# Kernel optimization log

Hardware: AMD Instinct MI355X
Metric: run time of the kernel (lower is better)

Reference implementation:

```python
import jax, jax.numpy as jnp
import numpy as np

NBINS = 128
LOGSCALE = False


def setup_inputs() -> dict:
    key = jax.random.key(0)
    X = jax.random.normal(key, (2048, 32768), dtype=jnp.float32)
    return {"X": X}


def reference(X) -> jnp.ndarray:
    # Flatten all non-leading dims (mirrors X.view(len(X), -1))
    X = X.reshape(X.shape[0], -1)
    ns = X.shape[1]
    nfreqs = 2 * (NBINS - 1) + 1          # window length (255)
    hop = nfreqs // 2
    starts = jnp.arange(0, ns - nfreqs + 1, hop)          # [nwin]
    idx = starts[:, None] + jnp.arange(nfreqs)[None, :]    # [nwin, nfreqs]
    W = X[:, idx]                          # [ntrials, nwin, nfreqs] gathered windows
    # One batched rfft + fused |.|^2 and mean over windows (Welch average)
    S = jnp.mean(jnp.abs(jnp.fft.rfft(W, axis=-1)) ** 2, axis=1)  # [ntrials, NBINS]
    if LOGSCALE:
        S = jnp.log10(S)
    return S
```

## Files before the change

kernel.cpp:

```cpp
#include <hip/hip_runtime.h>
#include <hip/hip_bf16.h>

#define NS     32768
#define NROWS  2048
#define HOP    127
#define NW     257
#define NB     128
#define WTILE  16
#define NT     17
#define TWOPI_255 0.02463994236f

typedef _Float16 f16;
typedef __attribute__((ext_vector_type(8))) _Float16 f16x8;
typedef __attribute__((ext_vector_type(4))) float f32x4;

__device__ inline f32x4 load4u(const float* p) {
    f32x4 v;
    __builtin_memcpy(&v, p, 16);
    return v;
}

__global__ __launch_bounds__(256, 4)
void psd_kernel(const float* __restrict__ X, float* __restrict__ out) {
    const int row  = blockIdx.x;
    const int tid  = threadIdx.x;
    const int lane = tid & 63;
    const int cq   = tid >> 6;
    const int r16  = lane & 15;
    const int kg   = lane >> 4;
    const int is_sin = cq >> 1;

    __shared__ alignas(16) f16 atile[2][WTILE * 256];
    __shared__ float scol[256];

    const float* __restrict__ xrow = X + (size_t)row * NS;

    const int sw  = tid >> 4;
    const int sk0 = (tid & 15) * 8;

    f32x4 fva, fvb, rva, rvb;
    {
        const int b = sw * HOP;
        fva = load4u(xrow + b + sk0);
        fvb = load4u(xrow + b + sk0 + 4);
        rva = load4u(xrow + b + 248 - sk0);
        rvb = load4u(xrow + b + 252 - sk0);
    }

    f16x8 bfrag[4][4];
    #pragma unroll
    for (int nt = 0; nt < 4; ++nt) {
        const int comp = cq * 64 + nt * 16 + r16;
        const int f    = comp & 127;
        #pragma unroll
        for (int kk = 0; kk < 4; ++kk) {
            int m = (f * (kk * 32 + kg * 8)) % 255;
            f16x8 v;
            #pragma unroll
            for (int j = 0; j < 8; ++j) {
                const float ang = (float)m * TWOPI_255;
                const float s   = is_sin ? __sinf(ang) : __cosf(ang);
                v[j] = (f16)s;
                m += f; if (m >= 255) m -= 255;
            }
            bfrag[nt][kk] = v;
        }
    }

    const f16x8 z8 = {(f16)0,(f16)0,(f16)0,(f16)0,(f16)0,(f16)0,(f16)0,(f16)0};
    auto fold_write = [&](int buf, bool valid) {
        float yp[8], ym[8];
        #pragma unroll
        for (int j = 0; j < 8; ++j) {
            const float fj = (j < 4) ? fva[j] : fvb[j - 4];
            const int   pi = 7 - j;
            const float rj = (pi < 4) ? rva[pi] : rvb[pi - 4];
            yp[j] = fj + rj;
            ym[j] = fj - rj;
        }
        if (sk0 == 0) { yp[0] = fva[0]; ym[0] = 0.0f; }
        f16x8 h0, h1;
        #pragma unroll
        for (int j = 0; j < 8; ++j) { h0[j] = (f16)yp[j]; h1[j] = (f16)ym[j]; }
        if (!valid) { h0 = z8; h1 = z8; }
        char* wp = (char*)&atile[buf][0];
        const uint sb  = (uint)(sw * 512 + sk0 * 2);
        const uint swz = (uint)((sw & 7) << 4);
        *(f16x8*)(wp + (sb ^ swz))         = h0;
        *(f16x8*)(wp + ((sb + 256) ^ swz)) = h1;
    };

    fold_write(0, true);
    {
        const int b = (WTILE + sw) * HOP;
        fva = load4u(xrow + b + sk0);
        fvb = load4u(xrow + b + sk0 + 4);
        rva = load4u(xrow + b + 248 - sk0);
        rvb = load4u(xrow + b + 252 - sk0);
    }
    __syncthreads();

    float ssum[4] = {0.f, 0.f, 0.f, 0.f};
    const uint rswz  = (uint)((r16 & 7) << 4);
    const uint rbase = (uint)(r16 * 512 + is_sin * 256 + kg * 16);

    for (int mt = 0; mt < NT; ++mt) {
        const int cur = mt & 1;

        const char* ap = (const char*)&atile[cur][0];
        f32x4 acc0 = {0,0,0,0}, acc1 = {0,0,0,0}, acc2 = {0,0,0,0}, acc3 = {0,0,0,0};
        __builtin_amdgcn_s_setprio(1);
        #pragma unroll
        for (int kk = 0; kk < 4; ++kk) {
            const f16x8 af = *(const f16x8*)(ap + ((rbase + (uint)(kk * 64)) ^ rswz));
            acc0 = __builtin_amdgcn_mfma_f32_16x16x32_f16(af, bfrag[0][kk], acc0, 0, 0, 0);
            acc1 = __builtin_amdgcn_mfma_f32_16x16x32_f16(af, bfrag[1][kk], acc1, 0, 0, 0);
            acc2 = __builtin_amdgcn_mfma_f32_16x16x32_f16(af, bfrag[2][kk], acc2, 0, 0, 0);
            acc3 = __builtin_amdgcn_mfma_f32_16x16x32_f16(af, bfrag[3][kk], acc3, 0, 0, 0);
        }
        __builtin_amdgcn_s_setprio(0);
        #pragma unroll
        for (int r = 0; r < 4; ++r) {
            ssum[0] += acc0[r] * acc0[r];
            ssum[1] += acc1[r] * acc1[r];
            ssum[2] += acc2[r] * acc2[r];
            ssum[3] += acc3[r] * acc3[r];
        }

        if (mt < NT - 1) {
            const bool valid = ((mt + 1) * WTILE + sw) < NW;
            fold_write(cur ^ 1, valid);
        }
        if (mt < NT - 2) {
            const int w = (mt + 2) * WTILE + sw;
            int b = w * HOP; if (b > NS - 256) b = NS - 256;
            fva = load4u(xrow + b + sk0);
            fvb = load4u(xrow + b + sk0 + 4);
            rva = load4u(xrow + b + 248 - sk0);
            rvb = load4u(xrow + b + 252 - sk0);
        }
        __syncthreads();
    }

    #pragma unroll
    for (int nt = 0; nt < 4; ++nt) {
        float v = ssum[nt];
        v += __shfl_xor(v, 16, 64);
        v += __shfl_xor(v, 32, 64);
        if (kg == 0) scol[cq * 64 + nt * 16 + r16] = v;
    }
    __syncthreads();
    if (tid < NB) {
        out[(size_t)row * NB + tid] = (scol[tid] + scol[tid + NB]) * (1.0f / 257.0f);
    }
}

extern "C" void kernel_launch(void* const* d_in, const int* in_sizes, int n_in,
                              void* d_out, int out_size, void* d_ws, size_t ws_size,
                              hipStream_t stream) {
    const float* X = (const float*)d_in[0];
    float* out = (float*)d_out;
    (void)in_sizes; (void)n_in; (void)d_ws; (void)ws_size; (void)out_size;
    psd_kernel<<<dim3(NROWS), dim3(256), 0, stream>>>(X, out);
}
```

Baseline: 65.09 us.

## Prefetch next A fragments into registers and overlap fold with MFMA

Restructures the main loop so the next tile's fold and LDS write, the global prefetch and the barrier all happen before the current tile's MFMAs. The A fragments for the next tile are read into registers ahead of time, so the MFMAs run from registers while LDS traffic and global loads are in flight. The fold now converts to packed fp16 first and does the add and subtract in packed half precision, which slightly changes rounding. The full __syncthreads is replaced by an LDS-only waitcnt plus barrier, and the occupancy hint drops from 4 to 3 blocks to leave room for the extra registers.

```diff
diff --git a/kernel.cpp b/kernel.cpp
--- a/kernel.cpp
+++ b/kernel.cpp
@@ -11,6 +11,7 @@
 #define TWOPI_255 0.02463994236f
 
 typedef _Float16 f16;
+typedef __attribute__((ext_vector_type(2))) _Float16 f16x2;
 typedef __attribute__((ext_vector_type(8))) _Float16 f16x8;
 typedef __attribute__((ext_vector_type(4))) float f32x4;
 
@@ -20,7 +21,7 @@
     return v;
 }
 
-__global__ __launch_bounds__(256, 4)
+__global__ __launch_bounds__(256, 3)
 void psd_kernel(const float* __restrict__ X, float* __restrict__ out) {
     const int row  = blockIdx.x;
     const int tid  = threadIdx.x;
@@ -67,30 +68,43 @@
         }
     }
 
-    const f16x8 z8 = {(f16)0,(f16)0,(f16)0,(f16)0,(f16)0,(f16)0,(f16)0,(f16)0};
-    auto fold_write = [&](int buf, bool valid) {
-        float yp[8], ym[8];
-        #pragma unroll
-        for (int j = 0; j < 8; ++j) {
-            const float fj = (j < 4) ? fva[j] : fvb[j - 4];
-            const int   pi = 7 - j;
-            const float rj = (pi < 4) ? rva[pi] : rvb[pi - 4];
-            yp[j] = fj + rj;
-            ym[j] = fj - rj;
-        }
-        if (sk0 == 0) { yp[0] = fva[0]; ym[0] = 0.0f; }
+    char* const lds = (char*)&atile[0][0];
+
+    const uint swz = (uint)((sw & 7) << 4);
+    const uint wr0 = ((uint)(sw * 512 + sk0 * 2)) ^ swz;
+    const uint wr1 = ((uint)(sw * 512 + sk0 * 2 + 256)) ^ swz;
+    const uint rswz = (uint)((r16 & 7) << 4);
+    uint rd[4];
+    #pragma unroll
+    for (int kk = 0; kk < 4; ++kk)
+        rd[kk] = ((uint)(r16 * 512 + is_sin * 256 + kg * 16 + kk * 64)) ^ rswz;
+
+    auto fold_write = [&](char* wp, bool valid) {
         f16x8 h0, h1;
         #pragma unroll
-        for (int j = 0; j < 8; ++j) { h0[j] = (f16)yp[j]; h1[j] = (f16)ym[j]; }
-        if (!valid) { h0 = z8; h1 = z8; }
-        char* wp = (char*)&atile[buf][0];
-        const uint sb  = (uint)(sw * 512 + sk0 * 2);
-        const uint swz = (uint)((sw & 7) << 4);
-        *(f16x8*)(wp + (sb ^ swz))         = h0;
-        *(f16x8*)(wp + ((sb + 256) ^ swz)) = h1;
+        for (int q = 0; q < 4; ++q) {
+            const int j0 = 2 * q, j1 = 2 * q + 1;
+            const float f0 = (j0 < 4) ? fva[j0] : fvb[j0 - 4];
+            const float f1 = (j1 < 4) ? fva[j1] : fvb[j1 - 4];
+            const float r0 = (j0 < 4) ? rvb[3 - j0] : rva[7 - j0];
+            const float r1 = (j1 < 4) ? rvb[3 - j1] : rva[7 - j1];
+            const f16x2 fp = __builtin_bit_cast(f16x2, __builtin_amdgcn_cvt_pkrtz(f0, f1));
+            const f16x2 rp = __builtin_bit_cast(f16x2, __builtin_amdgcn_cvt_pkrtz(r0, r1));
+            const f16x2 s = fp + rp;
+            const f16x2 d = fp - rp;
+            h0[j0] = s[0]; h0[j1] = s[1];
+            h1[j0] = d[0]; h1[j1] = d[1];
+        }
+        if (sk0 == 0) { h0[0] = (f16)fva[0]; h1[0] = (f16)0.0f; }
+        if (!valid) {
+            #pragma unroll
+            for (int j = 0; j < 8; ++j) { h0[j] = (f16)0.0f; h1[j] = (f16)0.0f; }
+        }
+        *(f16x8*)(wp + wr0) = h0;
+        *(f16x8*)(wp + wr1) = h1;
     };
 
-    fold_write(0, true);
+    fold_write(lds, true);
     {
         const int b = (WTILE + sw) * HOP;
         fva = load4u(xrow + b + sk0);
@@ -98,25 +112,46 @@
         rva = load4u(xrow + b + 248 - sk0);
         rvb = load4u(xrow + b + 252 - sk0);
     }
-    __syncthreads();
+    asm volatile("s_waitcnt lgkmcnt(0)" ::: "memory");
+    __builtin_amdgcn_s_barrier();
+    asm volatile("" ::: "memory");
+
+    f16x8 acur[4], anxt[4];
+    #pragma unroll
+    for (int kk = 0; kk < 4; ++kk) acur[kk] = *(const f16x8*)(lds + rd[kk]);
 
     float ssum[4] = {0.f, 0.f, 0.f, 0.f};
-    const uint rswz  = (uint)((r16 & 7) << 4);
-    const uint rbase = (uint)(r16 * 512 + is_sin * 256 + kg * 16);
 
     for (int mt = 0; mt < NT; ++mt) {
-        const int cur = mt & 1;
+        if (mt < NT - 1) {
+            char* wp = lds + (((mt + 1) & 1) << 13);
+            const bool valid = ((mt + 1) * WTILE + sw) < NW;
+            fold_write(wp, valid);
+            if (mt < NT - 2) {
+                const int w = (mt + 2) * WTILE + sw;
+                int b = w * HOP; if (b > NS - 256) b = NS - 256;
+                fva = load4u(xrow + b + sk0);
+                fvb = load4u(xrow + b + sk0 + 4);
+                rva = load4u(xrow + b + 248 - sk0);
+                rvb = load4u(xrow + b + 252 - sk0);
+            }
+            asm volatile("s_waitcnt lgkmcnt(0)" ::: "memory");
+            __builtin_amdgcn_s_barrier();
+            asm volatile("" ::: "memory");
+            const char* ap = lds + (((mt + 1) & 1) << 13);
+            #pragma unroll
+            for (int kk = 0; kk < 4; ++kk)
+                anxt[kk] = *(const f16x8*)(ap + rd[kk]);
+        }
 
-        const char* ap = (const char*)&atile[cur][0];
         f32x4 acc0 = {0,0,0,0}, acc1 = {0,0,0,0}, acc2 = {0,0,0,0}, acc3 = {0,0,0,0};
         __builtin_amdgcn_s_setprio(1);
         #pragma unroll
         for (int kk = 0; kk < 4; ++kk) {
-            const f16x8 af = *(const f16x8*)(ap + ((rbase + (uint)(kk * 64)) ^ rswz));
-            acc0 = __builtin_amdgcn_mfma_f32_16x16x32_f16(af, bfrag[0][kk], acc0, 0, 0, 0);
-            acc1 = __builtin_amdgcn_mfma_f32_16x16x32_f16(af, bfrag[1][kk], acc1, 0, 0, 0);
-            acc2 = __builtin_amdgcn_mfma_f32_16x16x32_f16(af, bfrag[2][kk], acc2, 0, 0, 0);
-            acc3 = __builtin_amdgcn_mfma_f32_16x16x32_f16(af, bfrag[3][kk], acc3, 0, 0, 0);
+            acc0 = __builtin_amdgcn_mfma_f32_16x16x32_f16(acur[kk], bfrag[0][kk], acc0, 0, 0, 0);
+            acc1 = __builtin_amdgcn_mfma_f32_16x16x32_f16(acur[kk], bfrag[1][kk], acc1, 0, 0, 0);
+            acc2 = __builtin_amdgcn_mfma_f32_16x16x32_f16(acur[kk], bfrag[2][kk], acc2, 0, 0, 0);
+            acc3 = __builtin_amdgcn_mfma_f32_16x16x32_f16(acur[kk], bfrag[3][kk], acc3, 0, 0, 0);
         }
         __builtin_amdgcn_s_setprio(0);
         #pragma unroll
@@ -128,18 +163,9 @@
         }
 
         if (mt < NT - 1) {
-            const bool valid = ((mt + 1) * WTILE + sw) < NW;
-            fold_write(cur ^ 1, valid);
+            #pragma unroll
+            for (int kk = 0; kk < 4; ++kk) acur[kk] = anxt[kk];
         }
-        if (mt < NT - 2) {
-            const int w = (mt + 2) * WTILE + sw;
-            int b = w * HOP; if (b > NS - 256) b = NS - 256;
-            fva = load4u(xrow + b + sk0);
-            fvb = load4u(xrow + b + sk0 + 4);
-            rva = load4u(xrow + b + 248 - sk0);
-            rvb = load4u(xrow + b + 252 - sk0);
-        }
-        __syncthreads();
     }
 
     #pragma unroll
```

Result: faster. 61.83 us (-5.0%).
